# Performance work log

Measured on AMD Instinct MI355X. Metric: run time of the kernel, lower is better.

Reference implementation:

```python
import jax, jax.numpy as jnp
import numpy as np

B, S, H = 16, 1024, 768


def setup_inputs() -> dict:
    key = jax.random.key(0)
    ks = jax.random.split(key, 12)
    s = 1.0 / np.sqrt(H)
    return {
        "encoder_outputs": jax.random.normal(ks[0], (B, S, H), dtype=jnp.float32),
        "mask": jax.random.randint(ks[1], (B, S), 0, 2, dtype=jnp.int32),
        "Wq": jax.random.uniform(ks[2], (H, H), jnp.float32, -s, s),
        "bq": jnp.zeros((H,), jnp.float32),
        "Wk": jax.random.uniform(ks[3], (H, H), jnp.float32, -s, s),
        "bk": jnp.zeros((H,), jnp.float32),
        "Wv": jax.random.uniform(ks[4], (H, H), jnp.float32, -s, s),
        "bv": jnp.zeros((H,), jnp.float32),
        "W1": jax.random.uniform(ks[5], (H, H), jnp.float32, -s, s),
        "b1": jnp.zeros((H,), jnp.float32),
        "W2": jax.random.uniform(ks[6], (H, H), jnp.float32, -s, s),
        "b2": jnp.zeros((H,), jnp.float32),
    }


def reference(encoder_outputs, mask, Wq, bq, Wk, bk, Wv, bv, W1, b1, W2, b2):
    x = encoder_outputs  # [B, S, H]
    inv_sqrt_h = 1.0 / jnp.sqrt(jnp.asarray(H, x.dtype))
    # ReLU-gated query/key projections (dropout=0 -> identity)
    q = jax.nn.relu(jnp.einsum('bsh,oh->bso', x, Wq) + bq)
    k = jax.nn.relu(jnp.einsum('bsh,oh->bso', x, Wk) + bk)
    score = jnp.einsum('bsh,bth->bst', q, k) * inv_sqrt_h  # [B, S, S]
    v = jnp.einsum('bsh,oh->bso', x, Wv) + bv
    m = mask.astype(x.dtype)  # [B, S]
    new_mask = m[:, :, None] * m[:, None, :]  # outer product [B, S, S]
    score = score - (1.0 - new_mask) * 1e12
    w = jax.nn.softmax(score, axis=2) * new_mask
    out = jnp.einsum('bst,bth->bsh', w, v)
    # FFN residual
    h1 = jax.nn.relu(jnp.einsum('bsh,oh->bso', out, W1) + b1)
    out = jnp.einsum('bsh,oh->bso', h1, W2) + b2 + out
    return out
```

## Files before the change

### kernel.cpp

```cpp
#include <hip/hip_runtime.h>
#include <hip/hip_bf16.h>

typedef __bf16 bf16_t;
typedef __bf16 bf16x8 __attribute__((ext_vector_type(8)));
typedef __bf16 bf16x4 __attribute__((ext_vector_type(4)));
typedef float f32x4 __attribute__((ext_vector_type(4)));
typedef unsigned int u32;
typedef const __attribute__((address_space(1))) u32* gptr_t;
typedef __attribute__((address_space(3))) u32* lptr_t;

static constexpr int Bb = 16, Ss = 1024, Hh = 768;

__global__ __launch_bounds__(256) void compact_mask(
    const int* __restrict__ mask, int* __restrict__ tok, int* __restrict__ cnt)
{
    const int b = blockIdx.x;
    const int t = threadIdx.x;
    const int4 m4 = *(const int4*)&mask[(b << 10) + (t << 2)];
    const int c = (m4.x != 0) + (m4.y != 0) + (m4.z != 0) + (m4.w != 0);
    __shared__ int sb[256];
    sb[t] = c;
    __syncthreads();
    for (int off = 1; off < 256; off <<= 1) {
        int v = (t >= off) ? sb[t - off] : 0;
        __syncthreads();
        sb[t] += v;
        __syncthreads();
    }
    int p = sb[t] - c;
    int* tb = tok + (b << 10);
    if (m4.x) tb[p++] = (t << 2) + 0;
    if (m4.y) tb[p++] = (t << 2) + 1;
    if (m4.z) tb[p++] = (t << 2) + 2;
    if (m4.w) tb[p++] = (t << 2) + 3;
    if (t == 255) cnt[b] = sb[255];
}

__global__ __launch_bounds__(256) void cvt_all(
    const float* __restrict__ x,
    const float* __restrict__ w0, const float* __restrict__ w1,
    const float* __restrict__ w2, const float* __restrict__ w3,
    const float* __restrict__ w4,
    const float* __restrict__ bq, const float* __restrict__ bk,
    const float* __restrict__ bv,
    const float* __restrict__ b1, const float* __restrict__ b2,
    const int* __restrict__ tok, const int* __restrict__ cnt,
    bf16_t* __restrict__ xc, bf16_t* __restrict__ wdst, float* __restrict__ bdst,
    float* __restrict__ cvec)
{
    const int bx = blockIdx.x;
    const int t = threadIdx.x;
    if (bx < 2880) {
        int seg = bx / 576;
        const float* src = seg == 0 ? w0 : seg == 1 ? w1 : seg == 2 ? w2 : seg == 3 ? w3 : w4;
        int i = (bx % 576) * 256 + t;
        float4 v = ((const float4*)src)[i];
        bf16x4 o = { (bf16_t)v.x, (bf16_t)v.y, (bf16_t)v.z, (bf16_t)v.w };
        ((bf16x4*)(wdst + (long)seg * 589824))[i] = o;
    } else if (bx < 2889) {
        int i = (bx - 2880) * 256 + t;
        if (i < 2304)
            bdst[i] = i < 768 ? bq[i] : i < 1536 ? bk[i - 768] : bv[i - 1536];
    } else if (bx < 19273) {
        const int idx = bx - 2889;
        const int b = idx >> 10, j = idx & 1023;
        if (j < cnt[b] && t < 192) {
            const int s = tok[(b << 10) + j];
            float4 v = ((const float4*)(x + ((long)((b << 10) + s)) * 768))[t];
            bf16x4 o = { (bf16_t)v.x, (bf16_t)v.y, (bf16_t)v.z, (bf16_t)v.w };
            ((bf16x4*)(xc + ((long)((b << 10) + j)) * 768))[t] = o;
        }
    } else {
        const int o = ((bx - 19273) << 3) + (t >> 5);
        const int l = t & 31;
        const float* wr = w4 + (long)o * 768;
        float acc = 0.f;
        for (int h = l; h < 768; h += 32) acc += wr[h] * fmaxf(b1[h], 0.f);
#pragma unroll
        for (int off = 16; off; off >>= 1) acc += __shfl_down(acc, off, 32);
        if (l == 0) cvec[o] = acc + b2[o];
    }
}

__device__ __forceinline__ void async_cp16(const void* g, void* l)
{
    __builtin_amdgcn_global_load_lds((gptr_t)g, (lptr_t)l, 16, 0, 0);
}

enum { EG_QKV = 0, EG_SCORE_C = 1, EG_PV = 2, EG_FFN1 = 3, EG_FFN2 = 4 };

template <int EPI>
__global__ __launch_bounds__(256) void mfma_gemm(
    const bf16_t* __restrict__ A, const bf16_t* __restrict__ B,
    const float* __restrict__ bias, const bf16_t* __restrict__ resid,
    const int* __restrict__ tok, const int* __restrict__ cnt,
    void* __restrict__ Cout, bf16_t* __restrict__ out2, bf16_t* __restrict__ out3,
    int K, int lda, int ldb, long sA, long sB, float scale)
{
    const int bz = blockIdx.z;
    const int cb = cnt[bz];
    const int m0 = blockIdx.y * 128;
    const int n0 = blockIdx.x * 128;
    if (m0 >= cb) return;
    if constexpr (EPI == EG_SCORE_C) { if (n0 >= cb) return; }
    const int Kend = (EPI == EG_PV) ? ((cb + 31) & ~31) : K;

    __shared__ bf16_t Asl[128 * 32];
    __shared__ bf16_t Bsl[128 * 32];

    const int tid = threadIdx.x;
    const int wid = tid >> 6;
    const int lane = tid & 63;
    const int wm = wid & 1, wn = wid >> 1;

    const bf16_t* Ab = A + (long)bz * sA;
    const bf16_t* Bp = B + (long)bz * sB;

    const int srow = (wid << 4) + (lane >> 2);
    const int scol = ((lane & 3) ^ ((lane >> 3) & 3)) << 3;

    const bf16_t* pa0 = Ab + (long)(m0 + srow) * lda + scol;
    const bf16_t* pa1 = Ab + (long)(m0 + 64 + srow) * lda + scol;
    const bf16_t* pb0 = Bp + (long)(n0 + srow) * ldb + scol;
    const bf16_t* pb1 = Bp + (long)(n0 + 64 + srow) * ldb + scol;

    bf16_t* la = &Asl[wid << 9];
    bf16_t* lb = &Bsl[wid << 9];

    const int frag_off = ((lane & 15) << 5) + (((lane >> 4) ^ ((lane >> 1) & 3)) << 3);

    f32x4 acc[4][4] = {};

    for (int k0 = 0; k0 < Kend; k0 += 32) {
        async_cp16(pa0 + k0, la);
        async_cp16(pa1 + k0, la + 2048);
        async_cp16(pb0 + k0, lb);
        async_cp16(pb1 + k0, lb + 2048);
        __syncthreads();

        bf16x8 af[4], bfr[4];
#pragma unroll
        for (int i = 0; i < 4; i++)
            af[i] = *(const bf16x8*)&Asl[(((wm << 2) + i) << 9) + frag_off];
#pragma unroll
        for (int j = 0; j < 4; j++)
            bfr[j] = *(const bf16x8*)&Bsl[(((wn << 2) + j) << 9) + frag_off];
#pragma unroll
        for (int i = 0; i < 4; i++)
#pragma unroll
            for (int j = 0; j < 4; j++)
                acc[i][j] = __builtin_amdgcn_mfma_f32_16x16x32_bf16(af[i], bfr[j], acc[i][j], 0, 0, 0);
        __syncthreads();
    }

    const int mb_ = m0 + (wm << 6);
    const int nb_ = n0 + (wn << 6);
    const int colw = lane & 15;
    const int rowq = (lane >> 4) << 2;

    if constexpr (EPI == EG_QKV) {
        float bj[4];
#pragma unroll
        for (int j = 0; j < 4; j++) bj[j] = bias[nb_ + (j << 4) + colw];
        if (nb_ < 1536) {
            bf16_t* C = ((nb_ < 768) ? (bf16_t*)Cout : out2) + (long)bz * 786432;
            const int cbase = (nb_ < 768) ? nb_ : nb_ - 768;
#pragma unroll
            for (int i = 0; i < 4; i++)
#pragma unroll
                for (int j = 0; j < 4; j++)
#pragma unroll
                    for (int r = 0; r < 4; r++) {
                        int row = mb_ + (i << 4) + rowq + r;
                        int col = cbase + (j << 4) + colw;
                        C[(long)row * Hh + col] = (bf16_t)fmaxf(acc[i][j][r] + bj[j], 0.f);
                    }
        } else {
            bf16_t* C = out3 + (long)bz * 786432;
#pragma unroll
            for (int i = 0; i < 4; i++) {
                const int jc0 = mb_ + (i << 4) + rowq;
#pragma unroll
                for (int j = 0; j < 4; j++) {
                    const int col = nb_ - 1536 + (j << 4) + colw;
                    bf16x4 o = { (bf16_t)(acc[i][j][0] + bj[j]), (bf16_t)(acc[i][j][1] + bj[j]),
                                 (bf16_t)(acc[i][j][2] + bj[j]), (bf16_t)(acc[i][j][3] + bj[j]) };
                    *(bf16x4*)&C[(long)col * 1024 + jc0] = o;
                }
            }
        }
    } else if constexpr (EPI == EG_SCORE_C) {
        bf16_t* C = (bf16_t*)Cout + (long)bz * 1048576;
#pragma unroll
        for (int i = 0; i < 4; i++) {
            const int kbase = mb_ + (i << 4) + rowq;
#pragma unroll
            for (int j = 0; j < 4; j++) {
                const int qrow = nb_ + (j << 4) + colw;
                bf16x4 o = { (bf16_t)(acc[i][j][0] * scale), (bf16_t)(acc[i][j][1] * scale),
                             (bf16_t)(acc[i][j][2] * scale), (bf16_t)(acc[i][j][3] * scale) };
                *(bf16x4*)&C[(long)qrow * 1024 + kbase] = o;
            }
        }
    } else if constexpr (EPI == EG_FFN2) {
        float* outp = (float*)Cout;
        const bf16_t* crow = resid + (long)bz * 786432;
        const int* tb = tok + (bz << 10);
        float bj[4];
#pragma unroll
        for (int j = 0; j < 4; j++) bj[j] = bias[nb_ + (j << 4) + colw];
#pragma unroll
        for (int i = 0; i < 4; i++)
#pragma unroll
            for (int r = 0; r < 4; r++) {
                const int jq = mb_ + (i << 4) + rowq + r;
                if (jq < cb) {
                    const int s = tb[jq];
                    float* orow = outp + ((long)((bz << 10) + s)) * 768;
                    const bf16_t* cr = crow + (long)jq * 768;
#pragma unroll
                    for (int j = 0; j < 4; j++) {
                        const int col = nb_ + (j << 4) + colw;
                        orow[col] = acc[i][j][r] + bj[j] + (float)cr[col];
                    }
                }
            }
    } else {
        bf16_t* C = (bf16_t*)Cout + (long)bz * 786432;
        float bj[4] = {0.f, 0.f, 0.f, 0.f};
        if constexpr (EPI == EG_FFN1) {
#pragma unroll
            for (int j = 0; j < 4; j++) bj[j] = bias[nb_ + (j << 4) + colw];
        }
#pragma unroll
        for (int i = 0; i < 4; i++)
#pragma unroll
            for (int j = 0; j < 4; j++)
#pragma unroll
                for (int r = 0; r < 4; r++) {
                    int row = mb_ + (i << 4) + rowq + r;
                    int col = nb_ + (j << 4) + colw;
                    float v = acc[i][j][r] + bj[j];
                    if constexpr (EPI == EG_FFN1) v = fmaxf(v, 0.f);
                    C[(long)row * Hh + col] = (bf16_t)v;
                }
    }
}

__global__ __launch_bounds__(256) void softmax_rows(
    bf16_t* __restrict__ S_, const int* __restrict__ cnt,
    const int* __restrict__ mask, const float* __restrict__ cvec,
    float* __restrict__ out)
{
    const int b = blockIdx.y;
    const int t = threadIdx.x;

    if (blockIdx.z == 1) {
        const int s = blockIdx.x;
        if (t >= 192 || mask[(b << 10) + s]) return;
        float4 v = ((const float4*)cvec)[t];
        ((float4*)(out + ((long)((b << 10) + s)) * 768))[t] = v;
        return;
    }

    const int jq = blockIdx.x;
    const int cb = cnt[b];
    if (jq >= cb) return;
    bf16_t* p = S_ + (((long)(b << 10)) + jq) * 1024;
    const int t0 = t << 2;

    bf16x4 v4 = *(const bf16x4*)&p[t0];
    float v0 = (t0 + 0 < cb) ? (float)v4[0] : -1e30f;
    float v1 = (t0 + 1 < cb) ? (float)v4[1] : -1e30f;
    float v2 = (t0 + 2 < cb) ? (float)v4[2] : -1e30f;
    float v3 = (t0 + 3 < cb) ? (float)v4[3] : -1e30f;

    float mx = fmaxf(fmaxf(v0, v1), fmaxf(v2, v3));
#pragma unroll
    for (int off = 32; off; off >>= 1) mx = fmaxf(mx, __shfl_down(mx, off, 64));
    __shared__ float redm[4], reds[4];
    if ((t & 63) == 0) redm[t >> 6] = mx;
    __syncthreads();
    mx = fmaxf(fmaxf(redm[0], redm[1]), fmaxf(redm[2], redm[3]));

    float e0 = __expf(v0 - mx), e1 = __expf(v1 - mx);
    float e2 = __expf(v2 - mx), e3 = __expf(v3 - mx);
    float sm = e0 + e1 + e2 + e3;
#pragma unroll
    for (int off = 32; off; off >>= 1) sm += __shfl_down(sm, off, 64);
    if ((t & 63) == 0) reds[t >> 6] = sm;
    __syncthreads();
    sm = reds[0] + reds[1] + reds[2] + reds[3];

    const float inv = 1.f / sm;
    bf16x4 o = { (bf16_t)(e0 * inv), (bf16_t)(e1 * inv),
                 (bf16_t)(e2 * inv), (bf16_t)(e3 * inv) };
    *(bf16x4*)&p[t0] = o;
}

extern "C" void kernel_launch(void* const* d_in, const int* in_sizes, int n_in,
                              void* d_out, int out_size, void* d_ws, size_t ws_size,
                              hipStream_t stream)
{
    const float* x  = (const float*)d_in[0];
    const int* mask = (const int*)d_in[1];
    const float* Wq = (const float*)d_in[2];
    const float* bq = (const float*)d_in[3];
    const float* Wk = (const float*)d_in[4];
    const float* bk = (const float*)d_in[5];
    const float* Wv = (const float*)d_in[6];
    const float* bv = (const float*)d_in[7];
    const float* W1 = (const float*)d_in[8];
    const float* b1 = (const float*)d_in[9];
    const float* W2 = (const float*)d_in[10];
    const float* b2 = (const float*)d_in[11];
    float* out = (float*)d_out;

    char* w = (char*)d_ws;
    bf16_t* xc   = (bf16_t*)(w + 0);
    bf16_t* qc   = (bf16_t*)(w + 25165824);
    bf16_t* kc   = (bf16_t*)(w + 50331648);
    bf16_t* vTc  = (bf16_t*)(w + 75497472);
    bf16_t* sc   = (bf16_t*)(w + 100663296);
    bf16_t* wqkv = (bf16_t*)(w + 134217728);
    bf16_t* w1b  = (bf16_t*)(w + 137756672);
    bf16_t* w2b  = (bf16_t*)(w + 138936320);
    float*  bqkv = (float*) (w + 140115968);
    int*    tok  = (int*)   (w + 140125184);
    int*    cnt  = (int*)   (w + 140190720);
    float*  cvec = (float*) (w + 140190784);
    bf16_t* ctxc = xc;
    bf16_t* h1c  = qc;

    const float inv_sqrt_h = 0.036084391824351615f;
    dim3 blk(256);

    compact_mask<<<16, blk, 0, stream>>>(mask, tok, cnt);
    cvt_all<<<19369, blk, 0, stream>>>(x, Wq, Wk, Wv, W1, W2, bq, bk, bv, b1, b2,
                                       tok, cnt, xc, wqkv, bqkv, cvec);

    mfma_gemm<EG_QKV><<<dim3(18, 8, 16), blk, 0, stream>>>(
        xc, wqkv, bqkv, nullptr, tok, cnt, qc, kc, vTc,
        768, 768, 768, 786432, 0, 1.f);

    mfma_gemm<EG_SCORE_C><<<dim3(8, 8, 16), blk, 0, stream>>>(
        kc, qc, nullptr, nullptr, tok, cnt, sc, nullptr, nullptr,
        768, 768, 768, 786432, 786432, inv_sqrt_h);

    softmax_rows<<<dim3(1024, 16, 2), blk, 0, stream>>>(sc, cnt, mask, cvec, out);

    mfma_gemm<EG_PV><<<dim3(6, 8, 16), blk, 0, stream>>>(
        sc, vTc, nullptr, nullptr, tok, cnt, ctxc, nullptr, nullptr,
        0, 1024, 1024, 1048576, 786432, 1.f);

    mfma_gemm<EG_FFN1><<<dim3(6, 8, 16), blk, 0, stream>>>(
        ctxc, w1b, b1, nullptr, tok, cnt, h1c, nullptr, nullptr,
        768, 768, 768, 786432, 0, 1.f);

    mfma_gemm<EG_FFN2><<<dim3(6, 8, 16), blk, 0, stream>>>(
        h1c, w2b, b2, ctxc, tok, cnt, out, nullptr, nullptr,
        768, 768, 768, 786432, 0, 1.f);
}
```

Before: 329.3 us.

## Double-buffer GEMM LDS staging and use 64x64 tiles for smaller GEMMs

```diff
diff --git a/kernel.cpp b/kernel.cpp
--- a/kernel.cpp
+++ b/kernel.cpp
@@ -89,7 +89,7 @@
 
 enum { EG_QKV = 0, EG_SCORE_C = 1, EG_PV = 2, EG_FFN1 = 3, EG_FFN2 = 4 };
 
-template <int EPI>
+template <int EPI, int BM, int BN>
 __global__ __launch_bounds__(256) void mfma_gemm(
     const bf16_t* __restrict__ A, const bf16_t* __restrict__ B,
     const float* __restrict__ bias, const bf16_t* __restrict__ resid,
@@ -99,14 +99,18 @@
 {
     const int bz = blockIdx.z;
     const int cb = cnt[bz];
-    const int m0 = blockIdx.y * 128;
-    const int n0 = blockIdx.x * 128;
+    const int m0 = blockIdx.y * BM;
+    const int n0 = blockIdx.x * BN;
     if (m0 >= cb) return;
     if constexpr (EPI == EG_SCORE_C) { if (n0 >= cb) return; }
     const int Kend = (EPI == EG_PV) ? ((cb + 31) & ~31) : K;
 
-    __shared__ bf16_t Asl[128 * 32];
-    __shared__ bf16_t Bsl[128 * 32];
+    constexpr int PM = BM / 2, PN = BN / 2;
+    constexpr int MI = PM / 16, NI = PN / 16;
+    constexpr int ASZ = BM * 32, BSZ = BN * 32;
+
+    __shared__ bf16_t Asl[2 * ASZ];
+    __shared__ bf16_t Bsl[2 * BSZ];
 
     const int tid = threadIdx.x;
     const int wid = tid >> 6;
@@ -124,51 +128,63 @@
     const bf16_t* pb0 = Bp + (long)(n0 + srow) * ldb + scol;
     const bf16_t* pb1 = Bp + (long)(n0 + 64 + srow) * ldb + scol;
 
-    bf16_t* la = &Asl[wid << 9];
-    bf16_t* lb = &Bsl[wid << 9];
+    const int woff = wid << 9;
 
     const int frag_off = ((lane & 15) << 5) + (((lane >> 4) ^ ((lane >> 1) & 3)) << 3);
 
-    f32x4 acc[4][4] = {};
-
+    f32x4 acc[MI][NI] = {};
+
+    auto stage = [&](int kk, int buf) {
+        bf16_t* la = &Asl[buf * ASZ + woff];
+        bf16_t* lb = &Bsl[buf * BSZ + woff];
+        async_cp16(pa0 + kk, la);
+        if constexpr (BM == 128) async_cp16(pa1 + kk, la + 2048);
+        async_cp16(pb0 + kk, lb);
+        if constexpr (BN == 128) async_cp16(pb1 + kk, lb + 2048);
+    };
+
+    stage(0, 0);
+    __syncthreads();
+
+    int cur = 0;
     for (int k0 = 0; k0 < Kend; k0 += 32) {
-        async_cp16(pa0 + k0, la);
-        async_cp16(pa1 + k0, la + 2048);
-        async_cp16(pb0 + k0, lb);
-        async_cp16(pb1 + k0, lb + 2048);
+        const int k1 = k0 + 32;
+        if (k1 < Kend) stage(k1, cur ^ 1);
+
+        const int cba = cur * ASZ, cbb = cur * BSZ;
+        bf16x8 af[MI], bfr[NI];
+#pragma unroll
+        for (int i = 0; i < MI; i++)
+            af[i] = *(const bf16x8*)&Asl[cba + ((wm * MI + i) << 9) + frag_off];
+#pragma unroll
+        for (int j = 0; j < NI; j++)
+            bfr[j] = *(const bf16x8*)&Bsl[cbb + ((wn * NI + j) << 9) + frag_off];
+#pragma unroll
+        for (int i = 0; i < MI; i++)
+#pragma unroll
+            for (int j = 0; j < NI; j++)
+                acc[i][j] = __builtin_amdgcn_mfma_f32_16x16x32_bf16(af[i], bfr[j], acc[i][j], 0, 0, 0);
+
         __syncthreads();
-
-        bf16x8 af[4], bfr[4];
-#pragma unroll
-        for (int i = 0; i < 4; i++)
-            af[i] = *(const bf16x8*)&Asl[(((wm << 2) + i) << 9) + frag_off];
-#pragma unroll
-        for (int j = 0; j < 4; j++)
-            bfr[j] = *(const bf16x8*)&Bsl[(((wn << 2) + j) << 9) + frag_off];
-#pragma unroll
-        for (int i = 0; i < 4; i++)
-#pragma unroll
-            for (int j = 0; j < 4; j++)
-                acc[i][j] = __builtin_amdgcn_mfma_f32_16x16x32_bf16(af[i], bfr[j], acc[i][j], 0, 0, 0);
-        __syncthreads();
-    }
-
-    const int mb_ = m0 + (wm << 6);
-    const int nb_ = n0 + (wn << 6);
+        cur ^= 1;
+    }
+
+    const int mb_ = m0 + wm * PM;
+    const int nb_ = n0 + wn * PN;
     const int colw = lane & 15;
     const int rowq = (lane >> 4) << 2;
 
     if constexpr (EPI == EG_QKV) {
-        float bj[4];
-#pragma unroll
-        for (int j = 0; j < 4; j++) bj[j] = bias[nb_ + (j << 4) + colw];
+        float bj[NI];
+#pragma unroll
+        for (int j = 0; j < NI; j++) bj[j] = bias[nb_ + (j << 4) + colw];
         if (nb_ < 1536) {
             bf16_t* C = ((nb_ < 768) ? (bf16_t*)Cout : out2) + (long)bz * 786432;
             const int cbase = (nb_ < 768) ? nb_ : nb_ - 768;
 #pragma unroll
-            for (int i = 0; i < 4; i++)
-#pragma unroll
-                for (int j = 0; j < 4; j++)
+            for (int i = 0; i < MI; i++)
+#pragma unroll
+                for (int j = 0; j < NI; j++)
 #pragma unroll
                     for (int r = 0; r < 4; r++) {
                         int row = mb_ + (i << 4) + rowq + r;
@@ -178,10 +194,10 @@
         } else {
             bf16_t* C = out3 + (long)bz * 786432;
 #pragma unroll
-            for (int i = 0; i < 4; i++) {
+            for (int i = 0; i < MI; i++) {
                 const int jc0 = mb_ + (i << 4) + rowq;
 #pragma unroll
-                for (int j = 0; j < 4; j++) {
+                for (int j = 0; j < NI; j++) {
                     const int col = nb_ - 1536 + (j << 4) + colw;
                     bf16x4 o = { (bf16_t)(acc[i][j][0] + bj[j]), (bf16_t)(acc[i][j][1] + bj[j]),
                                  (bf16_t)(acc[i][j][2] + bj[j]), (bf16_t)(acc[i][j][3] + bj[j]) };
@@ -192,10 +208,10 @@
     } else if constexpr (EPI == EG_SCORE_C) {
         bf16_t* C = (bf16_t*)Cout + (long)bz * 1048576;
 #pragma unroll
-        for (int i = 0; i < 4; i++) {
+        for (int i = 0; i < MI; i++) {
             const int kbase = mb_ + (i << 4) + rowq;
 #pragma unroll
-            for (int j = 0; j < 4; j++) {
+            for (int j = 0; j < NI; j++) {
                 const int qrow = nb_ + (j << 4) + colw;
                 bf16x4 o = { (bf16_t)(acc[i][j][0] * scale), (bf16_t)(acc[i][j][1] * scale),
                              (bf16_t)(acc[i][j][2] * scale), (bf16_t)(acc[i][j][3] * scale) };
@@ -206,11 +222,11 @@
         float* outp = (float*)Cout;
         const bf16_t* crow = resid + (long)bz * 786432;
         const int* tb = tok + (bz << 10);
-        float bj[4];
-#pragma unroll
-        for (int j = 0; j < 4; j++) bj[j] = bias[nb_ + (j << 4) + colw];
-#pragma unroll
-        for (int i = 0; i < 4; i++)
+        float bj[NI];
+#pragma unroll
+        for (int j = 0; j < NI; j++) bj[j] = bias[nb_ + (j << 4) + colw];
+#pragma unroll
+        for (int i = 0; i < MI; i++)
 #pragma unroll
             for (int r = 0; r < 4; r++) {
                 const int jq = mb_ + (i << 4) + rowq + r;
@@ -219,7 +235,7 @@
                     float* orow = outp + ((long)((bz << 10) + s)) * 768;
                     const bf16_t* cr = crow + (long)jq * 768;
 #pragma unroll
-                    for (int j = 0; j < 4; j++) {
+                    for (int j = 0; j < NI; j++) {
                         const int col = nb_ + (j << 4) + colw;
                         orow[col] = acc[i][j][r] + bj[j] + (float)cr[col];
                     }
@@ -227,15 +243,17 @@
             }
     } else {
         bf16_t* C = (bf16_t*)Cout + (long)bz * 786432;
-        float bj[4] = {0.f, 0.f, 0.f, 0.f};
+        float bj[NI];
+#pragma unroll
+        for (int j = 0; j < NI; j++) bj[j] = 0.f;
         if constexpr (EPI == EG_FFN1) {
 #pragma unroll
-            for (int j = 0; j < 4; j++) bj[j] = bias[nb_ + (j << 4) + colw];
+            for (int j = 0; j < NI; j++) bj[j] = bias[nb_ + (j << 4) + colw];
         }
 #pragma unroll
-        for (int i = 0; i < 4; i++)
-#pragma unroll
-            for (int j = 0; j < 4; j++)
+        for (int i = 0; i < MI; i++)
+#pragma unroll
+            for (int j = 0; j < NI; j++)
 #pragma unroll
                 for (int r = 0; r < 4; r++) {
                     int row = mb_ + (i << 4) + rowq + r;
@@ -339,25 +357,25 @@
     cvt_all<<<19369, blk, 0, stream>>>(x, Wq, Wk, Wv, W1, W2, bq, bk, bv, b1, b2,
                                        tok, cnt, xc, wqkv, bqkv, cvec);
 
-    mfma_gemm<EG_QKV><<<dim3(18, 8, 16), blk, 0, stream>>>(
+    mfma_gemm<EG_QKV, 128, 128><<<dim3(18, 8, 16), blk, 0, stream>>>(
         xc, wqkv, bqkv, nullptr, tok, cnt, qc, kc, vTc,
         768, 768, 768, 786432, 0, 1.f);
 
-    mfma_gemm<EG_SCORE_C><<<dim3(8, 8, 16), blk, 0, stream>>>(
+    mfma_gemm<EG_SCORE_C, 64, 64><<<dim3(16, 16, 16), blk, 0, stream>>>(
         kc, qc, nullptr, nullptr, tok, cnt, sc, nullptr, nullptr,
         768, 768, 768, 786432, 786432, inv_sqrt_h);
 
     softmax_rows<<<dim3(1024, 16, 2), blk, 0, stream>>>(sc, cnt, mask, cvec, out);
 
-    mfma_gemm<EG_PV><<<dim3(6, 8, 16), blk, 0, stream>>>(
+    mfma_gemm<EG_PV, 64, 64><<<dim3(12, 16, 16), blk, 0, stream>>>(
         sc, vTc, nullptr, nullptr, tok, cnt, ctxc, nullptr, nullptr,
         0, 1024, 1024, 1048576, 786432, 1.f);
 
-    mfma_gemm<EG_FFN1><<<dim3(6, 8, 16), blk, 0, stream>>>(
+    mfma_gemm<EG_FFN1, 64, 64><<<dim3(12, 16, 16), blk, 0, stream>>>(
         ctxc, w1b, b1, nullptr, tok, cnt, h1c, nullptr, nullptr,
         768, 768, 768, 786432, 0, 1.f);
 
-    mfma_gemm<EG_FFN2><<<dim3(6, 8, 16), blk, 0, stream>>>(
+    mfma_gemm<EG_FFN2, 64, 64><<<dim3(12, 16, 16), blk, 0, stream>>>(
         h1c, w2b, b2, ctxc, tok, cnt, out, nullptr, nullptr,
         768, 768, 768, 786432, 0, 1.f);
 }
```

New measurement: 338.2 us. 2.7% more time.

## Rewrite MFMA GEMM as 256x256 tile, 8-wave, double-buffered ping-pong pipeline

Applied to the files above, without the earlier changes.

```diff
diff --git a/kernel.cpp b/kernel.cpp
--- a/kernel.cpp
+++ b/kernel.cpp
@@ -89,72 +89,131 @@
 
 enum { EG_QKV = 0, EG_SCORE_C = 1, EG_PV = 2, EG_FFN1 = 3, EG_FFN2 = 4 };
 
+#define SBAR asm volatile("s_barrier" ::: "memory")
+#define LGK0 do { asm volatile("s_waitcnt lgkmcnt(0)" ::: "memory"); \
+                  __builtin_amdgcn_sched_barrier(0); } while (0)
+#define VMW(n) asm volatile("s_waitcnt vmcnt(" #n ")" ::: "memory")
+
+#define RD_A(dst, buf, mh) do { _Pragma("unroll") \
+  for (int _i = 0; _i < 4; _i++) { \
+    const char* _p = Ac + (buf)*32768 + ((wm*128 + ((mh)*4+_i)*16 + arow) << 7); \
+    dst[_i][0] = *(const bf16x8*)(_p + ck0); \
+    dst[_i][1] = *(const bf16x8*)(_p + ck1); } } while (0)
+
+#define RD_B(dst, buf, nh) do { _Pragma("unroll") \
+  for (int _j = 0; _j < 2; _j++) { \
+    const char* _p = Bc + (buf)*32768 + ((wn*64 + ((nh)*2+_j)*16 + arow) << 7); \
+    dst[_j][0] = *(const bf16x8*)(_p + ck0); \
+    dst[_j][1] = *(const bf16x8*)(_p + ck1); } } while (0)
+
+#define MQ(afv, bfv, mh, nh) do { __builtin_amdgcn_s_setprio(1); _Pragma("unroll") \
+  for (int _i = 0; _i < 4; _i++) { _Pragma("unroll") \
+    for (int _j = 0; _j < 2; _j++) { \
+      acc[(mh)*4+_i][(nh)*2+_j] = __builtin_amdgcn_mfma_f32_16x16x32_bf16( \
+          afv[_i][0], bfv[_j][0], acc[(mh)*4+_i][(nh)*2+_j], 0, 0, 0); \
+      acc[(mh)*4+_i][(nh)*2+_j] = __builtin_amdgcn_mfma_f32_16x16x32_bf16( \
+          afv[_i][1], bfv[_j][1], acc[(mh)*4+_i][(nh)*2+_j], 0, 0, 0); } } \
+  __builtin_amdgcn_s_setprio(0); } while (0)
+
+#define ST_A(buf, h, tk) do { \
+  async_cp16(pAs[h][0] + (long)(tk)*64, &Asl[(buf)*16384 + ((h)*128 + wid*8)*64]); \
+  async_cp16(pAs[h][1] + (long)(tk)*64, &Asl[(buf)*16384 + ((h)*128 + 64 + wid*8)*64]); } while (0)
+#define ST_B(buf, h, tk) do { \
+  async_cp16(pBs[h][0] + (long)(tk)*64, &Bsl[(buf)*16384 + ((h)*128 + wid*8)*64]); \
+  async_cp16(pBs[h][1] + (long)(tk)*64, &Bsl[(buf)*16384 + ((h)*128 + 64 + wid*8)*64]); } while (0)
+
 template <int EPI>
-__global__ __launch_bounds__(256) void mfma_gemm(
+__global__ __launch_bounds__(512, 2) void mfma_gemm(
     const bf16_t* __restrict__ A, const bf16_t* __restrict__ B,
     const float* __restrict__ bias, const bf16_t* __restrict__ resid,
     const int* __restrict__ tok, const int* __restrict__ cnt,
     void* __restrict__ Cout, bf16_t* __restrict__ out2, bf16_t* __restrict__ out3,
     int K, int lda, int ldb, long sA, long sB, float scale)
 {
-    const int bz = blockIdx.z;
+    const int gx = gridDim.x, gy = gridDim.y;
+    const int nwg = gx * gy * gridDim.z;
+    int lid = blockIdx.x + gx * (blockIdx.y + gy * blockIdx.z);
+    lid = (lid & 7) * (nwg >> 3) + (lid >> 3);
+    const int bxs = lid % gx;
+    const int tmp = lid / gx;
+    const int bys = tmp % gy;
+    const int bz  = tmp / gy;
+
     const int cb = cnt[bz];
-    const int m0 = blockIdx.y * 128;
-    const int n0 = blockIdx.x * 128;
+    const int m0 = bys << 8;
+    const int n0 = bxs << 8;
     if (m0 >= cb) return;
     if constexpr (EPI == EG_SCORE_C) { if (n0 >= cb) return; }
-    const int Kend = (EPI == EG_PV) ? ((cb + 31) & ~31) : K;
-
-    __shared__ bf16_t Asl[128 * 32];
-    __shared__ bf16_t Bsl[128 * 32];
+    const int Kend = (EPI == EG_PV) ? ((cb + 127) & ~127) : K;
+    const int niter = Kend >> 7;
+
+    __shared__ __align__(16) bf16_t Asl[2 * 16384];
+    __shared__ __align__(16) bf16_t Bsl[2 * 16384];
 
     const int tid = threadIdx.x;
     const int wid = tid >> 6;
     const int lane = tid & 63;
-    const int wm = wid & 1, wn = wid >> 1;
+    const int wm = wid >> 2, wn = wid & 3;
 
     const bf16_t* Ab = A + (long)bz * sA;
     const bf16_t* Bp = B + (long)bz * sB;
 
-    const int srow = (wid << 4) + (lane >> 2);
-    const int scol = ((lane & 3) ^ ((lane >> 3) & 3)) << 3;
-
-    const bf16_t* pa0 = Ab + (long)(m0 + srow) * lda + scol;
-    const bf16_t* pa1 = Ab + (long)(m0 + 64 + srow) * lda + scol;
-    const bf16_t* pb0 = Bp + (long)(n0 + srow) * ldb + scol;
-    const bf16_t* pb1 = Bp + (long)(n0 + 64 + srow) * ldb + scol;
-
-    bf16_t* la = &Asl[wid << 9];
-    bf16_t* lb = &Bsl[wid << 9];
-
-    const int frag_off = ((lane & 15) << 5) + (((lane >> 4) ^ ((lane >> 1) & 3)) << 3);
-
-    f32x4 acc[4][4] = {};
-
-    for (int k0 = 0; k0 < Kend; k0 += 32) {
-        async_cp16(pa0 + k0, la);
-        async_cp16(pa1 + k0, la + 2048);
-        async_cp16(pb0 + k0, lb);
-        async_cp16(pb1 + k0, lb + 2048);
-        __syncthreads();
-
-        bf16x8 af[4], bfr[4];
-#pragma unroll
-        for (int i = 0; i < 4; i++)
-            af[i] = *(const bf16x8*)&Asl[(((wm << 2) + i) << 9) + frag_off];
-#pragma unroll
-        for (int j = 0; j < 4; j++)
-            bfr[j] = *(const bf16x8*)&Bsl[(((wn << 2) + j) << 9) + frag_off];
-#pragma unroll
-        for (int i = 0; i < 4; i++)
-#pragma unroll
-            for (int j = 0; j < 4; j++)
-                acc[i][j] = __builtin_amdgcn_mfma_f32_16x16x32_bf16(af[i], bfr[j], acc[i][j], 0, 0, 0);
-        __syncthreads();
+    const int srow8 = lane >> 3;
+    const int scg = ((lane & 7) ^ srow8) << 3;
+
+    const bf16_t* pAs[2][2];
+    const bf16_t* pBs[2][2];
+#pragma unroll
+    for (int h = 0; h < 2; h++)
+#pragma unroll
+        for (int q = 0; q < 2; q++) {
+            pAs[h][q] = Ab + (long)(m0 + h*128 + q*64 + wid*8 + srow8) * lda + scg;
+            pBs[h][q] = Bp + (long)(n0 + h*128 + q*64 + wid*8 + srow8) * ldb + scg;
+        }
+
+    const int arow = lane & 15;
+    const int ck0 = (((lane >> 4)    ) ^ (lane & 7)) << 4;
+    const int ck1 = (((lane >> 4) + 4) ^ (lane & 7)) << 4;
+    const char* Ac = (const char*)Asl;
+    const char* Bc = (const char*)Bsl;
+
+    f32x4 acc[8][4] = {};
+    bf16x8 afA[4][2], afC[4][2], bfA[2][2], bfB[2][2];
+
+    ST_B(0, 0, 0); ST_B(0, 1, 0); ST_A(0, 0, 0); ST_A(0, 1, 0); ST_B(1, 0, 1);
+    __builtin_amdgcn_sched_barrier(0);
+    VMW(2); SBAR;
+
+    for (int it = 0; it < niter; ++it) {
+        const int t1 = 2 * it + 1;
+        const bool more = (it + 1 < niter);
+        RD_A(afA, 0, 0); RD_B(bfA, 0, 0);
+        ST_B(1, 1, t1);
+        SBAR; LGK0; MQ(afA, bfA, 0, 0); SBAR;
+        RD_B(bfB, 0, 1);
+        ST_A(1, 0, t1);
+        SBAR; LGK0; MQ(afA, bfB, 0, 1); SBAR;
+        RD_A(afC, 0, 1);
+        ST_A(1, 1, t1);
+        SBAR; LGK0; MQ(afC, bfA, 1, 0); SBAR;
+        if (more) { ST_B(0, 0, t1 + 1); __builtin_amdgcn_sched_barrier(0); VMW(2); }
+        else      { __builtin_amdgcn_sched_barrier(0); VMW(0); }
+        SBAR; MQ(afC, bfB, 1, 1); SBAR;
+        RD_A(afA, 1, 0); RD_B(bfA, 1, 0);
+        if (more) ST_B(0, 1, t1 + 1);
+        SBAR; LGK0; MQ(afA, bfA, 0, 0); SBAR;
+        RD_B(bfB, 1, 1);
+        if (more) ST_A(0, 0, t1 + 1);
+        SBAR; LGK0; MQ(afA, bfB, 0, 1); SBAR;
+        RD_A(afC, 1, 1);
+        if (more) ST_A(0, 1, t1 + 1);
+        SBAR; LGK0; MQ(afC, bfA, 1, 0); SBAR;
+        if (more) { ST_B(1, 0, t1 + 2); __builtin_amdgcn_sched_barrier(0); VMW(2); }
+        SBAR; MQ(afC, bfB, 1, 1); SBAR;
     }
 
-    const int mb_ = m0 + (wm << 6);
-    const int nb_ = n0 + (wn << 6);
+    const int mb_ = m0 + wm * 128;
+    const int nb_ = n0 + wn * 64;
     const int colw = lane & 15;
     const int rowq = (lane >> 4) << 2;
 
@@ -166,7 +225,7 @@
             bf16_t* C = ((nb_ < 768) ? (bf16_t*)Cout : out2) + (long)bz * 786432;
             const int cbase = (nb_ < 768) ? nb_ : nb_ - 768;
 #pragma unroll
-            for (int i = 0; i < 4; i++)
+            for (int i = 0; i < 8; i++)
 #pragma unroll
                 for (int j = 0; j < 4; j++)
 #pragma unroll
@@ -178,7 +237,7 @@
         } else {
             bf16_t* C = out3 + (long)bz * 786432;
 #pragma unroll
-            for (int i = 0; i < 4; i++) {
+            for (int i = 0; i < 8; i++) {
                 const int jc0 = mb_ + (i << 4) + rowq;
 #pragma unroll
                 for (int j = 0; j < 4; j++) {
@@ -192,7 +251,7 @@
     } else if constexpr (EPI == EG_SCORE_C) {
         bf16_t* C = (bf16_t*)Cout + (long)bz * 1048576;
 #pragma unroll
-        for (int i = 0; i < 4; i++) {
+        for (int i = 0; i < 8; i++) {
             const int kbase = mb_ + (i << 4) + rowq;
 #pragma unroll
             for (int j = 0; j < 4; j++) {
@@ -210,7 +269,7 @@
 #pragma unroll
         for (int j = 0; j < 4; j++) bj[j] = bias[nb_ + (j << 4) + colw];
 #pragma unroll
-        for (int i = 0; i < 4; i++)
+        for (int i = 0; i < 8; i++)
 #pragma unroll
             for (int r = 0; r < 4; r++) {
                 const int jq = mb_ + (i << 4) + rowq + r;
@@ -227,13 +286,15 @@
             }
     } else {
         bf16_t* C = (bf16_t*)Cout + (long)bz * 786432;
-        float bj[4] = {0.f, 0.f, 0.f, 0.f};
+        float bj[4];
+#pragma unroll
+        for (int j = 0; j < 4; j++) bj[j] = 0.f;
         if constexpr (EPI == EG_FFN1) {
 #pragma unroll
             for (int j = 0; j < 4; j++) bj[j] = bias[nb_ + (j << 4) + colw];
         }
 #pragma unroll
-        for (int i = 0; i < 4; i++)
+        for (int i = 0; i < 8; i++)
 #pragma unroll
             for (int j = 0; j < 4; j++)
 #pragma unroll
@@ -334,30 +395,31 @@
 
     const float inv_sqrt_h = 0.036084391824351615f;
     dim3 blk(256);
+    dim3 blk5(512);
 
     compact_mask<<<16, blk, 0, stream>>>(mask, tok, cnt);
     cvt_all<<<19369, blk, 0, stream>>>(x, Wq, Wk, Wv, W1, W2, bq, bk, bv, b1, b2,
                                        tok, cnt, xc, wqkv, bqkv, cvec);
 
-    mfma_gemm<EG_QKV><<<dim3(18, 8, 16), blk, 0, stream>>>(
+    mfma_gemm<EG_QKV><<<dim3(9, 4, 16), blk5, 0, stream>>>(
         xc, wqkv, bqkv, nullptr, tok, cnt, qc, kc, vTc,
         768, 768, 768, 786432, 0, 1.f);
 
-    mfma_gemm<EG_SCORE_C><<<dim3(8, 8, 16), blk, 0, stream>>>(
+    mfma_gemm<EG_SCORE_C><<<dim3(4, 4, 16), blk5, 0, stream>>>(
         kc, qc, nullptr, nullptr, tok, cnt, sc, nullptr, nullptr,
         768, 768, 768, 786432, 786432, inv_sqrt_h);
 
     softmax_rows<<<dim3(1024, 16, 2), blk, 0, stream>>>(sc, cnt, mask, cvec, out);
 
-    mfma_gemm<EG_PV><<<dim3(6, 8, 16), blk, 0, stream>>>(
+    mfma_gemm<EG_PV><<<dim3(3, 4, 16), blk5, 0, stream>>>(
         sc, vTc, nullptr, nullptr, tok, cnt, ctxc, nullptr, nullptr,
         0, 1024, 1024, 1048576, 786432, 1.f);
 
-    mfma_gemm<EG_FFN1><<<dim3(6, 8, 16), blk, 0, stream>>>(
+    mfma_gemm<EG_FFN1><<<dim3(3, 4, 16), blk5, 0, stream>>>(
         ctxc, w1b, b1, nullptr, tok, cnt, h1c, nullptr, nullptr,
         768, 768, 768, 786432, 0, 1.f);
 
-    mfma_gemm<EG_FFN2><<<dim3(6, 8, 16), blk, 0, stream>>>(
+    mfma_gemm<EG_FFN2><<<dim3(3, 4, 16), blk5, 0, stream>>>(
         h1c, w2b, b2, ctxc, tok, cnt, out, nullptr, nullptr,
         768, 768, 768, 786432, 0, 1.f);
 }
```

Result: no change. 329.9 us (+0.2%).
